# Kernel optimization log

Hardware: AMD Instinct MI355X
Metric: run time of the kernel (lower is better)

The kernel has to match this reference:

```python
import jax, jax.numpy as jnp
import numpy as np

B, T, A, K, STEPS, E = 2, 16384, 128, 128, 16, 126


def soft_dirac_last(x):
    # softmax forward-replaced by one-hot(argmax), straight-through backward
    sm = jax.nn.softmax(x, axis=-1)
    hard = jax.nn.one_hot(jnp.argmax(x, axis=-1), x.shape[-1], dtype=x.dtype)
    return sm + jax.lax.stop_gradient(hard - sm)


def _encode(x, d_unit, atom_embeddings):
    # x: (B,1,T); d_unit: (A,K) unit-norm atoms
    rng = jnp.linspace(0.0, 1.0, T, dtype=x.dtype)
    kernel = d_unit[:, None, :]  # OIH
    pad = [(K // 2, K - 1 - K // 2)]  # SAME
    batch_ix = jnp.arange(B)

    def step(res, _):
        # dense feature map: correlation of residual with every atom
        fm = jax.lax.conv_general_dilated(
            res, kernel, window_strides=(1,), padding=pad,
            dimension_numbers=("NCH", "OIH", "NCH"))  # (B,A,T)
        flat = fm.reshape(B, A * T)
        fi = jnp.argmax(flat, axis=-1)                      # sparsify n_to_keep=1
        value = jnp.take_along_axis(flat, fi[:, None], axis=-1)  # (B,1)
        ai = fi // T
        ti = fi % T
        # position: soft_dirac over time of sparse fm summed over atoms
        pos_row = jnp.zeros((B, T), x.dtype).at[batch_ix, ti].set(value[:, 0])
        pd = soft_dirac_last(pos_row)
        position = jnp.sum(pd * rng[None, :], axis=-1, keepdims=True) * 20.0  # (B,1)
        # atom one-hot: soft_dirac over atom axis of sparse fm summed over time
        atom_row = jnp.zeros((B, A), x.dtype).at[batch_ix, ai].set(value[:, 0])
        ad = soft_dirac_last(atom_row)
        ae = ad @ atom_embeddings  # (B,E)
        emb = jnp.concatenate([position, value, ae], axis=-1)  # (B, 2+E)
        # matching-pursuit residual update: subtract value * atom at found shift
        recon = value * d_unit[ai]  # (B,K)
        buf = jnp.zeros((B, T + K), x.dtype)
        buf = jax.vmap(lambda bb, rr, tt: jax.lax.dynamic_update_slice(bb, rr, (tt,)))(buf, recon, ti)
        res = res - buf[:, None, K // 2:K // 2 + T]
        return res, emb

    res, embs = jax.lax.scan(step, x, None, length=STEPS)
    embs = jnp.transpose(embs, (1, 0, 2))  # (B, STEPS, 2+E)
    return embs, res


def _canonical_ordering(embs, proj):
    keys = embs @ proj  # (B, STEPS)
    order = jnp.argsort(keys, axis=-1)
    return jnp.take_along_axis(embs, order[:, :, None], axis=1)


def setup_inputs() -> dict:
    key = jax.random.key(0)
    ks = jax.random.split(key, 5)
    return {
        "a": jax.random.normal(ks[0], (B, 1, T), jnp.float32),
        "b": jax.random.normal(ks[1], (B, 1, T), jnp.float32),
        "d": jax.random.normal(ks[2], (A, K), jnp.float32),
        "atom_embeddings": jax.random.normal(ks[3], (A, E), jnp.float32) * 0.1,
        "ordering_proj": jax.random.normal(ks[4], (128,), jnp.float32),
    }


def reference(a, b, d, atom_embeddings, ordering_proj):
    d_unit = d / (jnp.linalg.norm(d, axis=-1, keepdims=True) + 1e-8)
    ae, a_res = _encode(a, d_unit, atom_embeddings)
    be, b_res = _encode(b, d_unit, atom_embeddings)
    ae = _canonical_ordering(ae, ordering_proj)
    be = _canonical_ordering(be, ordering_proj)
    a_norm = jnp.linalg.norm(a_res.reshape(-1, T), axis=-1)
    b_norm = jnp.linalg.norm(b_res.reshape(-1, T), axis=-1)
    return jnp.mean((ae - be) ** 2) + jnp.mean(jnp.abs(a_norm - b_norm))
```

## Files before the change

kernel.cpp:

```cpp
#include <hip/hip_runtime.h>
#include <math.h>

#define T_DIM 16384
#define A_DIM 128
#define K_DIM 128
#define N_STEPS 16
#define E_DIM 126
#define NSEQ 4

#define ATI 16
#define TT 256
#define NPT 512
#define INC_B 32
#define HB 8192
#define RL_LEN 8319
#define RL_PAD 8608
#define SS_LEN 383
#define SS_PAD 404

#define PIDX(i) ((i) + ((i) >> 5))

__device__ inline unsigned long long pack_vi(float v, int fi) {
    unsigned int b = __float_as_uint(v);
    b = (b & 0x80000000u) ? ~b : (b | 0x80000000u);
    return ((unsigned long long)b << 32) | (unsigned int)(~fi);
}
__device__ inline void unpack_vi(unsigned long long p, float* v, int* fi) {
    unsigned int lo = (unsigned int)(p & 0xffffffffu);
    unsigned int b = (unsigned int)(p >> 32);
    unsigned int fb = (b & 0x80000000u) ? (b & 0x7fffffffu) : ~b;
    *v = __uint_as_float(fb);
    *fi = (int)(~lo);
}

__global__ __launch_bounds__(256) void k_prep(
    const float* __restrict__ d, const float* __restrict__ a,
    const float* __restrict__ b, float* __restrict__ du,
    float* __restrict__ res, int* __restrict__ cnt,
    unsigned long long* __restrict__ slots) {
    int blk = blockIdx.x, tid = threadIdx.x;
    if (blk < 128) {
        __shared__ float s[128];
        float v = 0.0f;
        if (tid < 128) { v = d[blk * K_DIM + tid]; s[tid] = v * v; }
        __syncthreads();
        for (int off = 64; off > 0; off >>= 1) {
            if (tid < off) s[tid] += s[tid + off];
            __syncthreads();
        }
        if (tid < 128) du[blk * K_DIM + tid] = v / (sqrtf(s[0]) + 1e-8f);
    } else if (blk < 384) {
        int i = (blk - 128) * 256 + tid;
        res[i] = (i < 2 * T_DIM) ? a[i] : b[i - 2 * T_DIM];
    } else {
        if (tid < NSEQ) cnt[tid] = 0;
        for (int i = tid; i < (N_STEPS - 1) * NSEQ * INC_B; i += 256) slots[i] = 0ULL;
    }
}

__device__ inline unsigned long long tile_compute(
    const float* __restrict__ duP, const float* __restrict__ rsh,
    int L0, int a_lo, int t_lo, int tid, unsigned long long* red4) {

    float acc[4][4];
    #pragma unroll
    for (int i = 0; i < 4; i++)
        #pragma unroll
        for (int j = 0; j < 4; j++) acc[i][j] = 0.0f;

    float r[8];
    #pragma unroll
    for (int m = 0; m < 8; m++) r[m] = rsh[PIDX(L0 + m)];

    #pragma unroll 4
    for (int k = 0; k < K_DIM; k += 4) {
        float dA[4][4];
        #pragma unroll
        for (int i = 0; i < 4; i++)
            *(float4*)dA[i] = *(const float4*)(duP + i * K_DIM + k);
        #pragma unroll
        for (int dk = 0; dk < 4; dk++) {
            #pragma unroll
            for (int i = 0; i < 4; i++) {
                float s = dA[i][dk];
                #pragma unroll
                for (int j = 0; j < 4; j++)
                    acc[i][j] = fmaf(s, r[j + dk], acc[i][j]);
            }
        }
        r[0] = r[4]; r[1] = r[5]; r[2] = r[6]; r[3] = r[7];
        #pragma unroll
        for (int m = 0; m < 4; m++) r[4 + m] = rsh[PIDX(L0 + k + 8 + m)];
    }

    float bv = -INFINITY;
    int bi = 0x7fffffff;
    #pragma unroll
    for (int i = 0; i < 4; i++) {
        int a = a_lo + i;
        #pragma unroll
        for (int j = 0; j < 4; j++) {
            int t = t_lo + j;
            int fi = a * T_DIM + t;
            float v = acc[i][j];
            if (v > bv || (v == bv && fi < bi)) { bv = v; bi = fi; }
        }
    }
    #pragma unroll
    for (int off = 32; off > 0; off >>= 1) {
        float v2 = __shfl_down(bv, off);
        int   i2 = __shfl_down(bi, off);
        if (v2 > bv || (v2 == bv && i2 < bi)) { bv = v2; bi = i2; }
    }
    if ((tid & 63) == 0) red4[tid >> 6] = pack_vi(bv, bi);
    __syncthreads();
    if (tid == 0) {
        unsigned long long m = red4[0];
        #pragma unroll
        for (int w = 1; w < 4; w++) if (red4[w] > m) m = red4[w];
        red4[0] = m;
    }
    __syncthreads();
    return red4[0];
}

__global__ __launch_bounds__(256) void k_step_full(
    float* __restrict__ res, const float* __restrict__ du,
    const float* __restrict__ ae, float* __restrict__ emb,
    unsigned long long* __restrict__ pmax, int* __restrict__ cnt,
    int* __restrict__ dirty0) {

    int seq = blockIdx.y;
    int blk = blockIdx.x;
    int a_base = (blk >> 6) * ATI;
    int t0 = (blk & 63) * TT;
    int tid = threadIdx.x;

    __shared__ float rsh[SS_PAD];
    __shared__ unsigned long long red4[4];
    __shared__ unsigned long long pm_sh[256];
    __shared__ int last_flag;

    const float* resS = res + seq * T_DIM;
    for (int i = tid; i < SS_LEN; i += 256) {
        int t = t0 - 64 + i;
        rsh[PIDX(i)] = (t >= 0 && t < T_DIM) ? resS[t] : 0.0f;
    }
    __syncthreads();

    int tg = tid & 63;
    int ag = __builtin_amdgcn_readfirstlane(tid >> 6);
    unsigned long long p = tile_compute(du + (a_base + ag * 4) * K_DIM, rsh,
                                        4 * tg, a_base + ag * 4, t0 + 4 * tg,
                                        tid, red4);
    if (tid == 0) {
        pmax[seq * NPT + blk] = p;
        __threadfence();
        last_flag = (atomicAdd(&cnt[seq], 1) == NPT - 1);
    }
    __syncthreads();
    if (!last_flag) return;

    __threadfence();
    {
        unsigned long long m0 = pmax[seq * NPT + tid];
        unsigned long long m1 = pmax[seq * NPT + 256 + tid];
        pm_sh[tid] = m0 > m1 ? m0 : m1;
    }
    __syncthreads();
    for (int off = 128; off > 0; off >>= 1) {
        if (tid < off) { if (pm_sh[tid + off] > pm_sh[tid]) pm_sh[tid] = pm_sh[tid + off]; }
        __syncthreads();
    }
    float value; int fi;
    unpack_vi(pm_sh[0], &value, &fi);
    int ai = fi >> 14;
    int ti = fi & (T_DIM - 1);
    int pos_idx = value > 0.0f ? ti : 0;
    int atom_idx = value > 0.0f ? ai : 0;

    float* e = emb + (seq * N_STEPS + 0) * 128;
    if (tid == 0) {
        e[0] = ((float)pos_idx / (float)(T_DIM - 1)) * 20.0f;
        e[1] = value;
        int nlo = ti - (K_DIM - 1); if (nlo < 0) nlo = 0;
        int nhi = ti + K_DIM;       if (nhi > T_DIM) nhi = T_DIM;
        dirty0[seq * 2 + 0] = nlo;
        dirty0[seq * 2 + 1] = nhi;
    }
    if (tid >= 2 && tid < 2 + E_DIM) e[tid] = ae[atom_idx * E_DIM + tid - 2];
    if (tid >= 128) {
        int k = tid - 128;
        int t = ti + k - K_DIM / 2;
        if (t >= 0 && t < T_DIM) {
            float r = res[seq * T_DIM + t];
            res[seq * T_DIM + t] = __fsub_rn(r, __fmul_rn(value, du[ai * K_DIM + k]));
        }
    }
}

__global__ __launch_bounds__(256) void k_inc(
    float* __restrict__ res, const float* __restrict__ du,
    const float* __restrict__ ae, float* __restrict__ emb,
    const unsigned long long* __restrict__ pmax,
    unsigned long long* __restrict__ slots, const int* __restrict__ dirty0) {

    int seq = blockIdx.y;
    int blk = blockIdx.x;
    int atile = blk >> 2;
    int half = (blk >> 1) & 1;
    int par = blk & 1;
    int a_base = atile * ATI;
    int base = half * HB;
    int tid = threadIdx.x;

    __shared__ float resL[RL_PAD];
    __shared__ unsigned long long red4[4];
    __shared__ unsigned long long tmax[16];
    __shared__ unsigned long long poll_sh[INC_B];
    __shared__ float val_s;
    __shared__ int   ti_s, ai_s, lo_sh, hi_sh;

    const float* resG = res + seq * T_DIM;
    for (int i4 = tid * 4; i4 < RL_LEN; i4 += 1024) {
        int t = base - 64 + i4;
        if (t >= 0 && t + 3 < T_DIM && i4 + 3 < RL_LEN) {
            float4 v = *(const float4*)&resG[t];
            resL[PIDX(i4 + 0)] = v.x; resL[PIDX(i4 + 1)] = v.y;
            resL[PIDX(i4 + 2)] = v.z; resL[PIDX(i4 + 3)] = v.w;
        } else {
            for (int m = 0; m < 4 && i4 + m < RL_LEN; m++) {
                int t2 = t + m;
                resL[PIDX(i4 + m)] = (t2 >= 0 && t2 < T_DIM) ? resG[t2] : 0.0f;
            }
        }
    }
    if (tid < 16) {
        int tt = half * 32 + par + 2 * tid;
        tmax[tid] = pmax[seq * NPT + atile * 64 + tt];
    }
    int lo = dirty0[seq * 2 + 0];
    int hi = dirty0[seq * 2 + 1];
    __syncthreads();

    for (int step = 1; step < N_STEPS; step++) {
        int T0 = lo >> 8;
        int cand = -1;
        if (((T0 & 1) == par) && ((T0 >> 5) == half)) cand = T0;
        int T1 = T0 + 1;
        if (T1 < 64 && ((T1 & 1) == par) && ((T1 >> 5) == half) && T1 * TT < hi)
            cand = T1;

        if (cand >= 0) {
            int t0 = cand * TT;
            int tg = tid & 63;
            int ag = __builtin_amdgcn_readfirstlane(tid >> 6);
            unsigned long long p = tile_compute(
                du + (a_base + ag * 4) * K_DIM, resL,
                (t0 - base) + 4 * tg, a_base + ag * 4, t0 + 4 * tg, tid, red4);
            if (tid == 0) tmax[(cand - half * 32 - par) >> 1] = p;
        }
        if (tid == 0) {
            unsigned long long m = tmax[0];
            for (int j = 1; j < 16; j++) if (tmax[j] > m) m = tmax[j];
            atomicExch(&slots[((step - 1) * NSEQ + seq) * INC_B + blk], m);
        }
        if (tid < INC_B) {
            const unsigned long long* sp =
                &slots[((step - 1) * NSEQ + seq) * INC_B + tid];
            unsigned long long v = __hip_atomic_load(sp, __ATOMIC_RELAXED,
                                                     __HIP_MEMORY_SCOPE_AGENT);
            while (v == 0ULL) {
                __builtin_amdgcn_s_sleep(1);
                v = __hip_atomic_load(sp, __ATOMIC_RELAXED,
                                      __HIP_MEMORY_SCOPE_AGENT);
            }
            poll_sh[tid] = v;
        }
        __syncthreads();
        if (tid == 0) {
            unsigned long long w = poll_sh[0];
            for (int j = 1; j < INC_B; j++) if (poll_sh[j] > w) w = poll_sh[j];
            float value; int fi;
            unpack_vi(w, &value, &fi);
            int ti = fi & (T_DIM - 1);
            val_s = value; ti_s = ti; ai_s = fi >> 14;
            int nlo = ti - (K_DIM - 1); if (nlo < 0) nlo = 0;
            int nhi = ti + K_DIM;       if (nhi > T_DIM) nhi = T_DIM;
            lo_sh = nlo; hi_sh = nhi;
        }
        __syncthreads();

        if (blk == 0) {
            float value = val_s;
            int ti = ti_s, ai = ai_s;
            int pos_idx = value > 0.0f ? ti : 0;
            int atom_idx = value > 0.0f ? ai : 0;
            float* e = emb + (seq * N_STEPS + step) * 128;
            if (tid == 0) {
                e[0] = ((float)pos_idx / (float)(T_DIM - 1)) * 20.0f;
                e[1] = value;
            }
            if (tid >= 2 && tid < 128) e[tid] = ae[atom_idx * E_DIM + tid - 2];
        }
        if (tid < 128) {
            int t = ti_s - K_DIM / 2 + tid;
            if (t >= 0 && t < T_DIM) {
                int L = t - base + 64;
                if (L >= 0 && L < RL_LEN) {
                    float r = resL[PIDX(L)];
                    resL[PIDX(L)] = __fsub_rn(r, __fmul_rn(val_s, du[ai_s * K_DIM + tid]));
                }
            }
        }
        __syncthreads();
        lo = lo_sh; hi = hi_sh;
    }

    if (atile == 0 && par == 0) {
        float* resW = res + seq * T_DIM + base;
        for (int t = tid; t < HB; t += 256) resW[t] = resL[PIDX(t + 64)];
    }
}

__global__ __launch_bounds__(1024) void k_tail(
    const float* __restrict__ res, const float* __restrict__ emb,
    const float* __restrict__ proj, float* __restrict__ out) {
    int tid = threadIdx.x;
    __shared__ float sh[1024];
    __shared__ float norms[NSEQ];
    __shared__ float keys[NSEQ][N_STEPS];
    __shared__ int   order[NSEQ][N_STEPS];

    {
        int seq = tid >> 8;
        int ln  = tid & 255;
        const float4* r4 = (const float4*)(res + seq * T_DIM);
        float s = 0.0f;
        #pragma unroll
        for (int j = 0; j < 16; j++) {
            float4 v = r4[j * 256 + ln];
            s = fmaf(v.x, v.x, s); s = fmaf(v.y, v.y, s);
            s = fmaf(v.z, v.z, s); s = fmaf(v.w, v.w, s);
        }
        sh[tid] = s;
        __syncthreads();
        for (int off = 128; off > 0; off >>= 1) {
            if (ln < off) sh[tid] += sh[tid + off];
            __syncthreads();
        }
        if (ln == 0) norms[seq] = sqrtf(sh[tid]);
        __syncthreads();
    }
    {
        int pair = tid >> 4;
        int seq = pair >> 4, st = pair & 15;
        int ln = tid & 15;
        const float* e = emb + (seq * N_STEPS + st) * 128 + ln * 8;
        const float* pr = proj + ln * 8;
        float kk = 0.0f;
        #pragma unroll
        for (int dd = 0; dd < 8; dd++) kk = fmaf(e[dd], pr[dd], kk);
        sh[tid] = kk;
        __syncthreads();
        for (int off = 8; off > 0; off >>= 1) {
            if (ln < off) sh[tid] += sh[tid + off];
            __syncthreads();
        }
        if (ln == 0) keys[seq][st] = sh[tid];
        __syncthreads();
    }
    if (tid < NSEQ) {
        int ord[N_STEPS];
        for (int i = 0; i < N_STEPS; i++) ord[i] = i;
        for (int i = 1; i < N_STEPS; i++) {
            int oi = ord[i];
            float kv = keys[tid][oi];
            int j = i - 1;
            while (j >= 0 && keys[tid][ord[j]] > kv) { ord[j + 1] = ord[j]; j--; }
            ord[j + 1] = oi;
        }
        for (int i = 0; i < N_STEPS; i++) order[tid][i] = ord[i];
    }
    __syncthreads();
    float s = 0.0f;
    #pragma unroll
    for (int t = 0; t < 4; t++) {
        int idx = tid + t * 1024;
        int b  = idx >> 11;
        int st = (idx >> 7) & 15;
        int dd = idx & 127;
        float va = emb[((b    ) * N_STEPS + order[b    ][st]) * 128 + dd];
        float vb = emb[((2 + b) * N_STEPS + order[2 + b][st]) * 128 + dd];
        float df = va - vb;
        s = fmaf(df, df, s);
    }
    sh[tid] = s;
    __syncthreads();
    for (int off = 512; off > 0; off >>= 1) {
        if (tid < off) sh[tid] += sh[tid + off];
        __syncthreads();
    }
    if (tid == 0) {
        float mse = sh[0] / 4096.0f;
        float mad = 0.5f * (fabsf(norms[0] - norms[2]) + fabsf(norms[1] - norms[3]));
        out[0] = mse + mad;
    }
}

extern "C" void kernel_launch(void* const* d_in, const int* in_sizes, int n_in,
                              void* d_out, int out_size, void* d_ws, size_t ws_size,
                              hipStream_t stream) {
    const float* a    = (const float*)d_in[0];
    const float* b    = (const float*)d_in[1];
    const float* d    = (const float*)d_in[2];
    const float* ae   = (const float*)d_in[3];
    const float* proj = (const float*)d_in[4];
    float* out = (float*)d_out;

    float* ws  = (float*)d_ws;
    float* res = ws;
    float* du  = res + NSEQ * T_DIM;
    float* emb = du + A_DIM * K_DIM;
    unsigned long long* pmax  = (unsigned long long*)(emb + NSEQ * N_STEPS * 128);
    unsigned long long* slots = pmax + NSEQ * NPT;
    int* cnt    = (int*)(slots + (N_STEPS - 1) * NSEQ * INC_B);
    int* dirty0 = cnt + NSEQ;

    k_prep<<<385, 256, 0, stream>>>(d, a, b, du, res, cnt, slots);

    dim3 gfull(NPT, NSEQ);
    k_step_full<<<gfull, 256, 0, stream>>>(res, du, ae, emb, pmax, cnt, dirty0);

    dim3 ginc(INC_B, NSEQ);
    k_inc<<<ginc, 256, 0, stream>>>(res, du, ae, emb, pmax, slots, dirty0);

    k_tail<<<1, 1024, 0, stream>>>(res, emb, proj, out);
}
```

Before: 243.8 us.

## Centralize per-step argmax in a coordinator block instead of all-to-all slot polling

Adds a dedicated coordinator block per sequence that holds the full 512-entry tile-max table, polls only the dirty tiles' new maxima, reduces the global argmax and publishes it through a single winner slot. Worker blocks now post their recomputed tile max directly and poll only that one slot. The old scheme had every worker poll 32 slots and do its own reduction. The goal is less cross-block polling traffic and less per-step synchronisation latency, at the cost of an extra serial hop through the coordinator. A block is added per sequence, and the design depends on all blocks being co-resident.

```diff
diff --git a/kernel.cpp b/kernel.cpp
--- a/kernel.cpp
+++ b/kernel.cpp
@@ -11,7 +11,7 @@
 #define ATI 16
 #define TT 256
 #define NPT 512
-#define INC_B 32
+#define NCB 32
 #define HB 8192
 #define RL_LEN 8319
 #define RL_PAD 8608
@@ -31,6 +31,10 @@
     unsigned int fb = (b & 0x80000000u) ? (b & 0x7fffffffu) : ~b;
     *v = __uint_as_float(fb);
     *fi = (int)(~lo);
+}
+
+__device__ inline unsigned long long u64max(unsigned long long a, unsigned long long b) {
+    return a > b ? a : b;
 }
 
 __global__ __launch_bounds__(256) void k_prep(
@@ -54,7 +58,8 @@
         res[i] = (i < 2 * T_DIM) ? a[i] : b[i - 2 * T_DIM];
     } else {
         if (tid < NSEQ) cnt[tid] = 0;
-        for (int i = tid; i < (N_STEPS - 1) * NSEQ * INC_B; i += 256) slots[i] = 0ULL;
+        for (int i = tid; i < (N_STEPS - 1) * NSEQ * 16 + (N_STEPS - 1) * NSEQ;
+             i += 256) slots[i] = 0ULL;
     }
 }
 
@@ -100,8 +105,7 @@
         int a = a_lo + i;
         #pragma unroll
         for (int j = 0; j < 4; j++) {
-            int t = t_lo + j;
-            int fi = a * T_DIM + t;
+            int fi = a * T_DIM + t_lo + j;
             float v = acc[i][j];
             if (v > bv || (v == bv && fi < bi)) { bv = v; bi = fi; }
         }
@@ -165,11 +169,11 @@
     {
         unsigned long long m0 = pmax[seq * NPT + tid];
         unsigned long long m1 = pmax[seq * NPT + 256 + tid];
-        pm_sh[tid] = m0 > m1 ? m0 : m1;
+        pm_sh[tid] = u64max(m0, m1);
     }
     __syncthreads();
     for (int off = 128; off > 0; off >>= 1) {
-        if (tid < off) { if (pm_sh[tid + off] > pm_sh[tid]) pm_sh[tid] = pm_sh[tid + off]; }
+        if (tid < off) pm_sh[tid] = u64max(pm_sh[tid], pm_sh[tid + off]);
         __syncthreads();
     }
     float value; int fi;
@@ -203,23 +207,82 @@
     float* __restrict__ res, const float* __restrict__ du,
     const float* __restrict__ ae, float* __restrict__ emb,
     const unsigned long long* __restrict__ pmax,
-    unsigned long long* __restrict__ slots, const int* __restrict__ dirty0) {
+    unsigned long long* __restrict__ dslots,
+    unsigned long long* __restrict__ wslots, const int* __restrict__ dirty0) {
 
     int seq = blockIdx.y;
     int blk = blockIdx.x;
+    int tid = threadIdx.x;
+
+    if (blk == NCB) {
+        __shared__ unsigned long long table[NPT];
+        __shared__ unsigned long long red4[4];
+        __shared__ unsigned long long wsh;
+        for (int i = tid; i < NPT; i += 256) table[i] = pmax[seq * NPT + i];
+        int lo = dirty0[seq * 2 + 0];
+        int hi = dirty0[seq * 2 + 1];
+        __syncthreads();
+
+        for (int step = 1; step < N_STEPS; step++) {
+            int T0 = lo >> 8, T1 = T0 + 1;
+            bool hasT1 = (T1 < 64) && (T1 * TT < hi);
+            if (tid < 16) {
+                int a = tid >> 1, w = tid & 1;
+                if (w == 0 || hasT1) {
+                    const unsigned long long* sp =
+                        &dslots[((step - 1) * NSEQ + seq) * 16 + tid];
+                    unsigned long long v = __hip_atomic_load(sp, __ATOMIC_RELAXED,
+                                                             __HIP_MEMORY_SCOPE_AGENT);
+                    while (v == 0ULL) {
+                        __builtin_amdgcn_s_sleep(1);
+                        v = __hip_atomic_load(sp, __ATOMIC_RELAXED,
+                                              __HIP_MEMORY_SCOPE_AGENT);
+                    }
+                    table[a * 64 + (w ? T1 : T0)] = v;
+                }
+            }
+            __syncthreads();
+            unsigned long long m = u64max(table[tid], table[tid + 256]);
+            #pragma unroll
+            for (int off = 32; off > 0; off >>= 1)
+                m = u64max(m, __shfl_down(m, off));
+            if ((tid & 63) == 0) red4[tid >> 6] = m;
+            __syncthreads();
+            if (tid == 0) {
+                unsigned long long w = red4[0];
+                #pragma unroll
+                for (int j = 1; j < 4; j++) w = u64max(w, red4[j]);
+                wsh = w;
+                atomicExch(&wslots[(step - 1) * NSEQ + seq], w);
+            }
+            __syncthreads();
+            float value; int fi;
+            unpack_vi(wsh, &value, &fi);
+            int ti = fi & (T_DIM - 1);
+            int ai = fi >> 14;
+            int pos_idx = value > 0.0f ? ti : 0;
+            int atom_idx = value > 0.0f ? ai : 0;
+            float* e = emb + (seq * N_STEPS + step) * 128;
+            if (tid == 0) {
+                e[0] = ((float)pos_idx / (float)(T_DIM - 1)) * 20.0f;
+                e[1] = value;
+            }
+            if (tid >= 2 && tid < 128) e[tid] = ae[atom_idx * E_DIM + tid - 2];
+            lo = ti - (K_DIM - 1); if (lo < 0) lo = 0;
+            hi = ti + K_DIM;       if (hi > T_DIM) hi = T_DIM;
+        }
+        return;
+    }
+
     int atile = blk >> 2;
     int half = (blk >> 1) & 1;
     int par = blk & 1;
     int a_base = atile * ATI;
     int base = half * HB;
-    int tid = threadIdx.x;
 
     __shared__ float resL[RL_PAD];
     __shared__ unsigned long long red4[4];
-    __shared__ unsigned long long tmax[16];
-    __shared__ unsigned long long poll_sh[INC_B];
-    __shared__ float val_s;
-    __shared__ int   ti_s, ai_s, lo_sh, hi_sh;
+    __shared__ unsigned long long wsh;
 
     const float* resG = res + seq * T_DIM;
     for (int i4 = tid * 4; i4 < RL_LEN; i4 += 1024) {
@@ -235,21 +298,16 @@
             }
         }
     }
-    if (tid < 16) {
-        int tt = half * 32 + par + 2 * tid;
-        tmax[tid] = pmax[seq * NPT + atile * 64 + tt];
-    }
     int lo = dirty0[seq * 2 + 0];
     int hi = dirty0[seq * 2 + 1];
     __syncthreads();
 
     for (int step = 1; step < N_STEPS; step++) {
-        int T0 = lo >> 8;
+        int T0 = lo >> 8, T1 = T0 + 1;
         int cand = -1;
         if (((T0 & 1) == par) && ((T0 >> 5) == half)) cand = T0;
-        int T1 = T0 + 1;
-        if (T1 < 64 && ((T1 & 1) == par) && ((T1 >> 5) == half) && T1 * TT < hi)
-            cand = T1;
+        else if (T1 < 64 && ((T1 & 1) == par) && ((T1 >> 5) == half) &&
+                 T1 * TT < hi) cand = T1;
 
         if (cand >= 0) {
             int t0 = cand * TT;
@@ -258,63 +316,39 @@
             unsigned long long p = tile_compute(
                 du + (a_base + ag * 4) * K_DIM, resL,
                 (t0 - base) + 4 * tg, a_base + ag * 4, t0 + 4 * tg, tid, red4);
-            if (tid == 0) tmax[(cand - half * 32 - par) >> 1] = p;
+            if (tid == 0)
+                atomicExch(&dslots[((step - 1) * NSEQ + seq) * 16 +
+                                   atile * 2 + (cand == T1 ? 1 : 0)], p);
         }
         if (tid == 0) {
-            unsigned long long m = tmax[0];
-            for (int j = 1; j < 16; j++) if (tmax[j] > m) m = tmax[j];
-            atomicExch(&slots[((step - 1) * NSEQ + seq) * INC_B + blk], m);
-        }
-        if (tid < INC_B) {
-            const unsigned long long* sp =
-                &slots[((step - 1) * NSEQ + seq) * INC_B + tid];
+            const unsigned long long* sp = &wslots[(step - 1) * NSEQ + seq];
             unsigned long long v = __hip_atomic_load(sp, __ATOMIC_RELAXED,
                                                      __HIP_MEMORY_SCOPE_AGENT);
             while (v == 0ULL) {
-                __builtin_amdgcn_s_sleep(1);
+                __builtin_amdgcn_s_sleep(2);
                 v = __hip_atomic_load(sp, __ATOMIC_RELAXED,
                                       __HIP_MEMORY_SCOPE_AGENT);
             }
-            poll_sh[tid] = v;
-        }
-        __syncthreads();
-        if (tid == 0) {
-            unsigned long long w = poll_sh[0];
-            for (int j = 1; j < INC_B; j++) if (poll_sh[j] > w) w = poll_sh[j];
-            float value; int fi;
-            unpack_vi(w, &value, &fi);
-            int ti = fi & (T_DIM - 1);
-            val_s = value; ti_s = ti; ai_s = fi >> 14;
-            int nlo = ti - (K_DIM - 1); if (nlo < 0) nlo = 0;
-            int nhi = ti + K_DIM;       if (nhi > T_DIM) nhi = T_DIM;
-            lo_sh = nlo; hi_sh = nhi;
-        }
-        __syncthreads();
-
-        if (blk == 0) {
-            float value = val_s;
-            int ti = ti_s, ai = ai_s;
-            int pos_idx = value > 0.0f ? ti : 0;
-            int atom_idx = value > 0.0f ? ai : 0;
-            float* e = emb + (seq * N_STEPS + step) * 128;
-            if (tid == 0) {
-                e[0] = ((float)pos_idx / (float)(T_DIM - 1)) * 20.0f;
-                e[1] = value;
-            }
-            if (tid >= 2 && tid < 128) e[tid] = ae[atom_idx * E_DIM + tid - 2];
-        }
+            wsh = v;
+        }
+        __syncthreads();
+        float value; int fi;
+        unpack_vi(wsh, &value, &fi);
+        int ti = fi & (T_DIM - 1);
+        int ai = fi >> 14;
         if (tid < 128) {
-            int t = ti_s - K_DIM / 2 + tid;
+            int t = ti - K_DIM / 2 + tid;
             if (t >= 0 && t < T_DIM) {
                 int L = t - base + 64;
                 if (L >= 0 && L < RL_LEN) {
                     float r = resL[PIDX(L)];
-                    resL[PIDX(L)] = __fsub_rn(r, __fmul_rn(val_s, du[ai_s * K_DIM + tid]));
+                    resL[PIDX(L)] = __fsub_rn(r, __fmul_rn(value, du[ai * K_DIM + tid]));
                 }
             }
         }
         __syncthreads();
-        lo = lo_sh; hi = hi_sh;
+        lo = ti - (K_DIM - 1); if (lo < 0) lo = 0;
+        hi = ti + K_DIM;       if (hi > T_DIM) hi = T_DIM;
     }
 
     if (atile == 0 && par == 0) {
@@ -422,18 +456,19 @@
     float* res = ws;
     float* du  = res + NSEQ * T_DIM;
     float* emb = du + A_DIM * K_DIM;
-    unsigned long long* pmax  = (unsigned long long*)(emb + NSEQ * N_STEPS * 128);
-    unsigned long long* slots = pmax + NSEQ * NPT;
-    int* cnt    = (int*)(slots + (N_STEPS - 1) * NSEQ * INC_B);
+    unsigned long long* pmax   = (unsigned long long*)(emb + NSEQ * N_STEPS * 128);
+    unsigned long long* dslots = pmax + NSEQ * NPT;
+    unsigned long long* wslots = dslots + (N_STEPS - 1) * NSEQ * 16;
+    int* cnt    = (int*)(wslots + (N_STEPS - 1) * NSEQ);
     int* dirty0 = cnt + NSEQ;
 
-    k_prep<<<385, 256, 0, stream>>>(d, a, b, du, res, cnt, slots);
+    k_prep<<<385, 256, 0, stream>>>(d, a, b, du, res, cnt, dslots);
 
     dim3 gfull(NPT, NSEQ);
     k_step_full<<<gfull, 256, 0, stream>>>(res, du, ae, emb, pmax, cnt, dirty0);
 
-    dim3 ginc(INC_B, NSEQ);
-    k_inc<<<ginc, 256, 0, stream>>>(res, du, ae, emb, pmax, slots, dirty0);
+    dim3 ginc(NCB + 1, NSEQ);
+    k_inc<<<ginc, 256, 0, stream>>>(res, du, ae, emb, pmax, dslots, wslots, dirty0);
 
     k_tail<<<1, 1024, 0, stream>>>(res, emb, proj, out);
 }
```

Result: faster. 235.1 us (-3.6%).
